# Optimization experiments

Hardware: AMD Instinct MI355X
Metric: run time of the kernel (lower is better)

Reference implementation:

```python
import jax, jax.numpy as jnp
import numpy as np

H = 8          # num heads
DK = 64        # d_model // H
D_MODEL = 512
WIN = 256


def setup_inputs() -> dict:
    key = jax.random.key(0)
    ks = jax.random.split(key, 12)
    B, S = 2, 2048
    mk = lambda k, shape, s=1.0: jax.random.normal(k, shape, dtype=jnp.float32) * s
    inp = {
        "query": mk(ks[0], (B, S, D_MODEL)),
        "key_in": mk(ks[1], (B, S, D_MODEL)),
        "value": mk(ks[2], (B, S, D_MODEL)),
        # nn.Linear(d_model, d_model) weights (out,in) and biases, x4
        "Wq": mk(ks[3], (D_MODEL, D_MODEL), 0.02), "bq": jnp.zeros((D_MODEL,), jnp.float32),
        "Wk": mk(ks[4], (D_MODEL, D_MODEL), 0.02), "bk": jnp.zeros((D_MODEL,), jnp.float32),
        "Wv": mk(ks[5], (D_MODEL, D_MODEL), 0.02), "bv": jnp.zeros((D_MODEL,), jnp.float32),
        "Wo": mk(ks[6], (D_MODEL, D_MODEL), 0.02), "bo": jnp.zeros((D_MODEL,), jnp.float32),
    }
    return inp


def reference(query, key_in, value, Wq, bq, Wk, bk, Wv, bv, Wo, bo):
    B, S, D = query.shape
    scale = np.float32(1.0 / np.sqrt(DK))

    def proj(x, W, b):
        # (B,S,D) -> (B,H,S,DK)
        return (x @ W.T + b).reshape(B, S, H, DK).transpose(0, 2, 1, 3)

    q = proj(query, Wq, bq)
    k = proj(key_in, Wk, bk)
    v = proj(value, Wv, bv)

    # Faithful to naive_masked_matmul: full (B,H,S,S) scores, with entries
    # OUTSIDE the sliding window left at exactly 0.0 (NOT -inf) before softmax.
    scores = jnp.einsum('bhid,bhjd->bhij', q, k) * scale
    idx = jnp.arange(S)
    band = jnp.abs(idx[:, None] - idx[None, :]) <= (WIN // 2)  # (S,S) bool
    scores = jnp.where(band, scores, jnp.float32(0.0))

    p_attn = jax.nn.softmax(scores, axis=-1)
    x = jnp.einsum('bhij,bhjd->bhid', p_attn, v)          # (B,H,S,DK)
    x = x.transpose(0, 2, 1, 3).reshape(B, S, D)          # (B,S,D)
    return x @ Wo.T + bo
```

## Files before the change

kernel.cpp:

```cpp
#include <hip/hip_runtime.h>
#include <hip/hip_bf16.h>

#define SS 2048
#define DD 512
#define HWIN 128

typedef __bf16 bf16x8 __attribute__((ext_vector_type(8)));
typedef unsigned short u16x8 __attribute__((ext_vector_type(8)));
typedef float f32x4 __attribute__((ext_vector_type(4)));

__device__ __forceinline__ unsigned short f2bf(float x) {
    unsigned u = __builtin_bit_cast(unsigned, x);
    return (unsigned short)((u + 0x7fffu + ((u >> 16) & 1u)) >> 16);
}
__device__ __forceinline__ float bf2f(unsigned short s) {
    unsigned u = ((unsigned)s) << 16;
    return __builtin_bit_cast(float, u);
}
__device__ __forceinline__ void split_bf(float x, unsigned short& h, unsigned short& l) {
    h = f2bf(x);
    l = f2bf(x - bf2f(h));
}
__device__ __forceinline__ void split8(float4 f0, float4 f1, u16x8& h, u16x8& l) {
    const float vals[8] = {f0.x, f0.y, f0.z, f0.w, f1.x, f1.y, f1.z, f1.w};
    #pragma unroll
    for (int i = 0; i < 8; ++i) {
        unsigned short hh, ll;
        split_bf(vals[i], hh, ll);
        h[i] = hh;
        l[i] = ll;
    }
}
__device__ __forceinline__ f32x4 mfma16(u16x8 a, u16x8 b, f32x4 c) {
    return __builtin_amdgcn_mfma_f32_16x16x32_bf16(
        __builtin_bit_cast(bf16x8, a), __builtin_bit_cast(bf16x8, b), c, 0, 0, 0);
}

template <bool A_FP32, bool OUT_SPLIT>
__device__ __forceinline__ void gemm_split_body(
    const float* __restrict__ Af,
    const unsigned short* __restrict__ AHg, const unsigned short* __restrict__ ALg,
    const float* __restrict__ W, const float* __restrict__ bias,
    unsigned short* __restrict__ OH, unsigned short* __restrict__ OL,
    float* __restrict__ OF)
{
    constexpr int K = 512, N = 512;
    __shared__ unsigned short Ah[8 * 64 * 8], Al[8 * 64 * 8];
    __shared__ unsigned short Bh[4 * 64 * 8], Bl[4 * 64 * 8];

    const int tid = threadIdx.x, wave = tid >> 6, lane = tid & 63;
    const int lm = lane & 15, lq = lane >> 4;
    const int m0 = blockIdx.y * 128, n0 = blockIdx.x * 64;
    const int wm = wave >> 1, wn = wave & 1;

    f32x4 acc[4][2] = {};

    const int ar0 = m0 + (wave * 2 + 0) * 16 + lm;
    const int ar1 = m0 + (wave * 2 + 1) * 16 + lm;
    const int br  = n0 + wave * 16 + lm;
    const int kb  = lq * 8;

    unsigned short* aD0h = &Ah[((wave * 2 + 0) * 64 + lane) * 8];
    unsigned short* aD1h = &Ah[((wave * 2 + 1) * 64 + lane) * 8];
    unsigned short* aD0l = &Al[((wave * 2 + 0) * 64 + lane) * 8];
    unsigned short* aD1l = &Al[((wave * 2 + 1) * 64 + lane) * 8];
    unsigned short* bDh  = &Bh[(wave * 64 + lane) * 8];
    unsigned short* bDl  = &Bl[(wave * 64 + lane) * 8];

    for (int k0 = 0; k0 < K; k0 += 32) {
        u16x8 a0h, a0l, a1h, a1l, b0h, b0l;
        if (A_FP32) {
            const float* p0 = Af + (size_t)ar0 * K + k0 + kb;
            split8(*(const float4*)p0, *(const float4*)(p0 + 4), a0h, a0l);
            const float* p1 = Af + (size_t)ar1 * K + k0 + kb;
            split8(*(const float4*)p1, *(const float4*)(p1 + 4), a1h, a1l);
        } else {
            a0h = *(const u16x8*)(AHg + (size_t)ar0 * K + k0 + kb);
            a0l = *(const u16x8*)(ALg + (size_t)ar0 * K + k0 + kb);
            a1h = *(const u16x8*)(AHg + (size_t)ar1 * K + k0 + kb);
            a1l = *(const u16x8*)(ALg + (size_t)ar1 * K + k0 + kb);
        }
        {
            const float* pw = W + (size_t)br * K + k0 + kb;
            split8(*(const float4*)pw, *(const float4*)(pw + 4), b0h, b0l);
        }
        __syncthreads();
        *(u16x8*)aD0h = a0h; *(u16x8*)aD0l = a0l;
        *(u16x8*)aD1h = a1h; *(u16x8*)aD1l = a1l;
        *(u16x8*)bDh  = b0h; *(u16x8*)bDl  = b0l;
        __syncthreads();

        u16x8 afh[4], afl[4], bfh[2], bfl[2];
        #pragma unroll
        for (int i = 0; i < 4; ++i) {
            afh[i] = *(const u16x8*)&Ah[((wm * 4 + i) * 64 + lane) * 8];
            afl[i] = *(const u16x8*)&Al[((wm * 4 + i) * 64 + lane) * 8];
        }
        #pragma unroll
        for (int j = 0; j < 2; ++j) {
            bfh[j] = *(const u16x8*)&Bh[((wn * 2 + j) * 64 + lane) * 8];
            bfl[j] = *(const u16x8*)&Bl[((wn * 2 + j) * 64 + lane) * 8];
        }
        #pragma unroll
        for (int i = 0; i < 4; ++i)
            #pragma unroll
            for (int j = 0; j < 2; ++j) {
                acc[i][j] = mfma16(afh[i], bfh[j], acc[i][j]);
                acc[i][j] = mfma16(afh[i], bfl[j], acc[i][j]);
                acc[i][j] = mfma16(afl[i], bfh[j], acc[i][j]);
            }
    }

    #pragma unroll
    for (int i = 0; i < 4; ++i)
        #pragma unroll
        for (int j = 0; j < 2; ++j) {
            const int col = n0 + (wn * 2 + j) * 16 + lm;
            const float bv = bias[col];
            #pragma unroll
            for (int r = 0; r < 4; ++r) {
                const int row = m0 + (wm * 4 + i) * 16 + lq * 4 + r;
                const float v = acc[i][j][r] + bv;
                if (OUT_SPLIT) {
                    unsigned short h, l;
                    split_bf(v, h, l);
                    OH[(size_t)row * N + col] = h;
                    OL[(size_t)row * N + col] = l;
                } else {
                    OF[(size_t)row * N + col] = v;
                }
            }
        }
}

__global__ __launch_bounds__(256) void proj_gemm(
    const float* __restrict__ q, const float* __restrict__ k, const float* __restrict__ v,
    const float* __restrict__ Wq, const float* __restrict__ Wk, const float* __restrict__ Wv,
    const float* __restrict__ bq, const float* __restrict__ bk, const float* __restrict__ bv,
    unsigned short* __restrict__ base)
{
    const int z = blockIdx.z;
    const float* A = (z == 0) ? q : ((z == 1) ? k : v);
    const float* W = (z == 0) ? Wq : ((z == 1) ? Wk : Wv);
    const float* bias = (z == 0) ? bq : ((z == 1) ? bk : bv);
    unsigned short* OH = base + (size_t)z * 4194304;
    unsigned short* OL = OH + 2097152;
    gemm_split_body<true, true>(A, nullptr, nullptr, W, bias, OH, OL, nullptr);
}

__global__ __launch_bounds__(256) void out_gemm(
    const unsigned short* __restrict__ XH, const unsigned short* __restrict__ XL,
    const float* __restrict__ Wo, const float* __restrict__ bo, float* __restrict__ O)
{
    gemm_split_body<false, false>(nullptr, XH, XL, Wo, bo, nullptr, nullptr, O);
}

__global__ __launch_bounds__(256) void vsum_stage1(
    const unsigned short* __restrict__ VH, const unsigned short* __restrict__ VL,
    float* __restrict__ partial)
{
    const int bh = blockIdx.x, c = blockIdx.y;
    const int h = bh & 7, b = bh >> 3;
    const int t = threadIdx.x, d = t & 63, g = t >> 6;
    __shared__ float p[4][64];
    const size_t base = ((size_t)b * SS + c * 64) * DD + (size_t)h * 64 + d;
    float acc = 0.f;
    #pragma unroll 4
    for (int s = g; s < 64; s += 4) {
        const size_t ix = base + (size_t)s * DD;
        acc += bf2f(VH[ix]) + bf2f(VL[ix]);
    }
    p[g][d] = acc;
    __syncthreads();
    if (t < 64)
        partial[((size_t)bh * 32 + c) * 64 + t] =
            p[0][t] + p[1][t] + p[2][t] + p[3][t];
}

__global__ __launch_bounds__(64) void vsum_stage2(
    const float* __restrict__ partial, float* __restrict__ VS)
{
    const int bh = blockIdx.x, d = threadIdx.x;
    float acc = 0.f;
    #pragma unroll 8
    for (int c = 0; c < 32; ++c)
        acc += partial[((size_t)bh * 32 + c) * 64 + d];
    VS[bh * 64 + d] = acc;
}

__global__ __launch_bounds__(256) void attn_mfma(
    const unsigned short* __restrict__ QH, const unsigned short* __restrict__ QL,
    const unsigned short* __restrict__ KH, const unsigned short* __restrict__ KL,
    const unsigned short* __restrict__ VH, const unsigned short* __restrict__ VL,
    const float* __restrict__ VS,
    unsigned short* __restrict__ XH, unsigned short* __restrict__ XL)
{
    const int bh = blockIdx.y, h = bh & 7, b = bh >> 3;
    const int i0 = blockIdx.x * 64;
    const int tid = threadIdx.x, wave = tid >> 6, lane = tid & 63;
    const int lm = lane & 15, lq = lane >> 4;
    const int kb = lq * 8;

    __shared__ unsigned short Kth[64][72], Ktl[64][72];
    __shared__ unsigned short Vth[64][72], Vtl[64][72];
    __shared__ unsigned short Swh[64][72], Swl[64][72];

    const size_t qoff = ((size_t)(b * SS + i0 + wave * 16 + lm)) * DD + h * 64 + kb;
    const u16x8 aQ0h = *(const u16x8*)(QH + qoff);
    const u16x8 aQ0l = *(const u16x8*)(QL + qoff);
    const u16x8 aQ1h = *(const u16x8*)(QH + qoff + 32);
    const u16x8 aQ1l = *(const u16x8*)(QL + qoff + 32);

    f32x4 oacc[4] = {};
    float dacc[4] = {0.f, 0.f, 0.f, 0.f};

    const int sr = tid & 63, sc = (tid >> 6) * 16;

    for (int jt = 0; jt < 5; ++jt) {
        const int jt0 = i0 - 128 + jt * 64;
        {
            const int j = jt0 + sr;
            u16x8 z = {0,0,0,0,0,0,0,0};
            u16x8 kh0 = z, kh1 = z, kl0 = z, kl1 = z;
            u16x8 vh0 = z, vh1 = z, vl0 = z, vl1 = z;
            if (j >= 0 && j < SS) {
                const size_t gb = ((size_t)(b * SS + j)) * DD + h * 64 + sc;
                kh0 = *(const u16x8*)(KH + gb); kh1 = *(const u16x8*)(KH + gb + 8);
                kl0 = *(const u16x8*)(KL + gb); kl1 = *(const u16x8*)(KL + gb + 8);
                vh0 = *(const u16x8*)(VH + gb); vh1 = *(const u16x8*)(VH + gb + 8);
                vl0 = *(const u16x8*)(VL + gb); vl1 = *(const u16x8*)(VL + gb + 8);
            }
            *(u16x8*)&Kth[sr][sc]     = kh0; *(u16x8*)&Kth[sr][sc + 8] = kh1;
            *(u16x8*)&Ktl[sr][sc]     = kl0; *(u16x8*)&Ktl[sr][sc + 8] = kl1;
            #pragma unroll
            for (int cc = 0; cc < 8; ++cc) {
                Vth[sc + cc][sr] = vh0[cc]; Vth[sc + 8 + cc][sr] = vh1[cc];
                Vtl[sc + cc][sr] = vl0[cc]; Vtl[sc + 8 + cc][sr] = vl1[cc];
            }
        }
        __syncthreads();

        #pragma unroll
        for (int js = 0; js < 4; ++js) {
            const int j0 = js * 16;
            const u16x8 bK0h = *(const u16x8*)&Kth[j0 + lm][kb];
            const u16x8 bK0l = *(const u16x8*)&Ktl[j0 + lm][kb];
            const u16x8 bK1h = *(const u16x8*)&Kth[j0 + lm][kb + 32];
            const u16x8 bK1l = *(const u16x8*)&Ktl[j0 + lm][kb + 32];
            f32x4 s = {0.f, 0.f, 0.f, 0.f};
            s = mfma16(aQ0h, bK0h, s);
            s = mfma16(aQ0h, bK0l, s);
            s = mfma16(aQ0l, bK0h, s);
            s = mfma16(aQ1h, bK1h, s);
            s = mfma16(aQ1h, bK1l, s);
            s = mfma16(aQ1l, bK1h, s);
            const int jg = jt0 + j0 + lm;
            const int iq = i0 + wave * 16 + lq * 4;
            #pragma unroll
            for (int r = 0; r < 4; ++r) {
                const int qi = iq + r;
                const bool in = (jg >= 0) && (jg < SS) &&
                                (jg >= qi - HWIN) && (jg <= qi + HWIN);
                const float w = in ? (__expf(s[r] * 0.125f) - 1.0f) : 0.0f;
                dacc[r] += w;
                unsigned short wh, wl;
                split_bf(w, wh, wl);
                Swh[wave * 16 + lq * 4 + r][j0 + lm] = wh;
                Swl[wave * 16 + lq * 4 + r][j0 + lm] = wl;
            }
        }
        __syncthreads();

        const u16x8 aP0h = *(const u16x8*)&Swh[wave * 16 + lm][kb];
        const u16x8 aP0l = *(const u16x8*)&Swl[wave * 16 + lm][kb];
        const u16x8 aP1h = *(const u16x8*)&Swh[wave * 16 + lm][kb + 32];
        const u16x8 aP1l = *(const u16x8*)&Swl[wave * 16 + lm][kb + 32];
        #pragma unroll
        for (int s4 = 0; s4 < 4; ++s4) {
            const u16x8 bV0h = *(const u16x8*)&Vth[s4 * 16 + lm][kb];
            const u16x8 bV0l = *(const u16x8*)&Vtl[s4 * 16 + lm][kb];
            const u16x8 bV1h = *(const u16x8*)&Vth[s4 * 16 + lm][kb + 32];
            const u16x8 bV1l = *(const u16x8*)&Vtl[s4 * 16 + lm][kb + 32];
            oacc[s4] = mfma16(aP0h, bV0h, oacc[s4]);
            oacc[s4] = mfma16(aP0l, bV0h, oacc[s4]);
            oacc[s4] = mfma16(aP0h, bV0l, oacc[s4]);
            oacc[s4] = mfma16(aP1h, bV1h, oacc[s4]);
            oacc[s4] = mfma16(aP1l, bV1h, oacc[s4]);
            oacc[s4] = mfma16(aP1h, bV1l, oacc[s4]);
        }
        __syncthreads();
    }

    #pragma unroll
    for (int r = 0; r < 4; ++r) {
        float v = dacc[r];
        v += __shfl_xor(v, 1);
        v += __shfl_xor(v, 2);
        v += __shfl_xor(v, 4);
        v += __shfl_xor(v, 8);
        dacc[r] = v + 2048.0f;
    }

    #pragma unroll
    for (int s4 = 0; s4 < 4; ++s4) {
        const float vsv = VS[bh * 64 + s4 * 16 + lm];
        #pragma unroll
        for (int r = 0; r < 4; ++r) {
            const int qrow = i0 + wave * 16 + lq * 4 + r;
            const float x = (oacc[s4][r] + vsv) / dacc[r];
            unsigned short xh, xl;
            split_bf(x, xh, xl);
            const size_t ix = ((size_t)(b * SS + qrow)) * DD + h * 64 + s4 * 16 + lm;
            XH[ix] = xh;
            XL[ix] = xl;
        }
    }
}

extern "C" void kernel_launch(void* const* d_in, const int* in_sizes, int n_in,
                              void* d_out, int out_size, void* d_ws, size_t ws_size,
                              hipStream_t stream)
{
    const float* query  = (const float*)d_in[0];
    const float* key_in = (const float*)d_in[1];
    const float* value  = (const float*)d_in[2];
    const float* Wq = (const float*)d_in[3]; const float* bq = (const float*)d_in[4];
    const float* Wk = (const float*)d_in[5]; const float* bk = (const float*)d_in[6];
    const float* Wv = (const float*)d_in[7]; const float* bv = (const float*)d_in[8];
    const float* Wo = (const float*)d_in[9]; const float* bo = (const float*)d_in[10];

    unsigned short* wsb = (unsigned short*)d_ws;
    unsigned short* QH = wsb;
    unsigned short* QL = wsb + 2097152;
    unsigned short* KH = wsb + 4194304;
    unsigned short* KL = wsb + 6291456;
    unsigned short* VH = wsb + 8388608;
    unsigned short* VL = wsb + 10485760;
    unsigned short* XH = wsb + 12582912;
    unsigned short* XL = wsb + 14680064;
    float* VSp = (float*)((char*)d_ws + 33554432);
    float* part = (float*)XH;

    proj_gemm<<<dim3(8, 32, 3), 256, 0, stream>>>(
        query, key_in, value, Wq, Wk, Wv, bq, bk, bv, QH);

    vsum_stage1<<<dim3(16, 32), 256, 0, stream>>>(VH, VL, part);
    vsum_stage2<<<16, 64, 0, stream>>>(part, VSp);

    attn_mfma<<<dim3(32, 16), 256, 0, stream>>>(
        QH, QL, KH, KL, VH, VL, VSp, XH, XL);

    out_gemm<<<dim3(8, 32), 256, 0, stream>>>(XH, XL, Wo, bo, (float*)d_out);
}
```

Before: 177.4 us.

## Pre-split projection weights once and remap block indices for XCD locality

Adds a castW kernel that splits Wq/Wk/Wv into interleaved bf16 hi/lo pairs once per call, so the projection GEMM loads pre-split weights instead of re-splitting fp32 weights in every block. All GEMM and attention launches move to flat 1D grids with an index remap that groups blocks sharing a weight tile or (batch, head) onto the same XCD via the round-robin dispatch, improving L2 reuse. This adds an extra kernel launch and workspace traffic, and relocates the partial-sum buffer inside the workspace.

Result: no change. 177.1 us (-0.1%).

```diff
diff --git a/kernel.cpp b/kernel.cpp
--- a/kernel.cpp
+++ b/kernel.cpp
@@ -36,13 +36,29 @@
         __builtin_bit_cast(bf16x8, a), __builtin_bit_cast(bf16x8, b), c, 0, 0, 0);
 }
 
-template <bool A_FP32, bool OUT_SPLIT>
+__global__ __launch_bounds__(256) void castW(
+    const float* __restrict__ wq, const float* __restrict__ wk,
+    const float* __restrict__ wv, unsigned short* __restrict__ dst)
+{
+    const size_t e0 = ((size_t)blockIdx.x * 256 + threadIdx.x) * 8;
+    const float* src; size_t off;
+    if      (e0 < 262144) { src = wq; off = e0; }
+    else if (e0 < 524288) { src = wk; off = e0 - 262144; }
+    else                  { src = wv; off = e0 - 524288; }
+    u16x8 h, l;
+    split8(*(const float4*)(src + off), *(const float4*)(src + off + 4), h, l);
+    *(u16x8*)(dst + 2 * e0)     = h;
+    *(u16x8*)(dst + 2 * e0 + 8) = l;
+}
+
+template <bool A_FP32, bool B_PAIRED, bool OUT_SPLIT>
 __device__ __forceinline__ void gemm_split_body(
     const float* __restrict__ Af,
     const unsigned short* __restrict__ AHg, const unsigned short* __restrict__ ALg,
-    const float* __restrict__ W, const float* __restrict__ bias,
+    const unsigned short* __restrict__ Wp, const float* __restrict__ Wf,
+    const float* __restrict__ bias,
     unsigned short* __restrict__ OH, unsigned short* __restrict__ OL,
-    float* __restrict__ OF)
+    float* __restrict__ OF, int m0, int n0)
 {
     constexpr int K = 512, N = 512;
     __shared__ unsigned short Ah[8 * 64 * 8], Al[8 * 64 * 8];
@@ -50,7 +66,6 @@
 
     const int tid = threadIdx.x, wave = tid >> 6, lane = tid & 63;
     const int lm = lane & 15, lq = lane >> 4;
-    const int m0 = blockIdx.y * 128, n0 = blockIdx.x * 64;
     const int wm = wave >> 1, wn = wave & 1;
 
     f32x4 acc[4][2] = {};
@@ -80,8 +95,12 @@
             a1h = *(const u16x8*)(AHg + (size_t)ar1 * K + k0 + kb);
             a1l = *(const u16x8*)(ALg + (size_t)ar1 * K + k0 + kb);
         }
-        {
-            const float* pw = W + (size_t)br * K + k0 + kb;
+        if (B_PAIRED) {
+            const unsigned short* pw = Wp + 2 * ((size_t)br * K + k0 + kb);
+            b0h = *(const u16x8*)pw;
+            b0l = *(const u16x8*)(pw + 8);
+        } else {
+            const float* pw = Wf + (size_t)br * K + k0 + kb;
             split8(*(const float4*)pw, *(const float4*)(pw + 4), b0h, b0l);
         }
         __syncthreads();
@@ -135,24 +154,35 @@
 
 __global__ __launch_bounds__(256) void proj_gemm(
     const float* __restrict__ q, const float* __restrict__ k, const float* __restrict__ v,
-    const float* __restrict__ Wq, const float* __restrict__ Wk, const float* __restrict__ Wv,
+    const unsigned short* __restrict__ WP,
     const float* __restrict__ bq, const float* __restrict__ bk, const float* __restrict__ bv,
     unsigned short* __restrict__ base)
 {
-    const int z = blockIdx.z;
+    const int d = blockIdx.x;
+    const int hi = d >> 6, low = d & 63;
+    const int x = low >> 3, r = low & 7;
+    const int g = hi * 8 + r;
+    const int y = g / 3, z = g - y * 3;
+
     const float* A = (z == 0) ? q : ((z == 1) ? k : v);
-    const float* W = (z == 0) ? Wq : ((z == 1) ? Wk : Wv);
+    const unsigned short* Wp = WP + (size_t)z * 524288;
     const float* bias = (z == 0) ? bq : ((z == 1) ? bk : bv);
     unsigned short* OH = base + (size_t)z * 4194304;
     unsigned short* OL = OH + 2097152;
-    gemm_split_body<true, true>(A, nullptr, nullptr, W, bias, OH, OL, nullptr);
+    gemm_split_body<true, true, true>(A, nullptr, nullptr, Wp, nullptr, bias,
+                                      OH, OL, nullptr, y * 128, x * 64);
 }
 
 __global__ __launch_bounds__(256) void out_gemm(
     const unsigned short* __restrict__ XH, const unsigned short* __restrict__ XL,
     const float* __restrict__ Wo, const float* __restrict__ bo, float* __restrict__ O)
 {
-    gemm_split_body<false, false>(nullptr, XH, XL, Wo, bo, nullptr, nullptr, O);
+    const int d = blockIdx.x;
+    const int hi = d >> 6, low = d & 63;
+    const int x = low >> 3, r = low & 7;
+    const int y = hi * 8 + r;
+    gemm_split_body<false, false, false>(nullptr, XH, XL, nullptr, Wo, bo,
+                                         nullptr, nullptr, O, y * 128, x * 64);
 }
 
 __global__ __launch_bounds__(256) void vsum_stage1(
@@ -195,8 +225,12 @@
     const float* __restrict__ VS,
     unsigned short* __restrict__ XH, unsigned short* __restrict__ XL)
 {
-    const int bh = blockIdx.y, h = bh & 7, b = bh >> 3;
-    const int i0 = blockIdx.x * 64;
+    const int dblk = blockIdx.x;
+    const int bhi = dblk >> 8, blow = dblk & 255;
+    const int xblk = blow >> 3, rr = blow & 7;
+    const int bh = bhi * 8 + rr;
+    const int h = bh & 7, b = bh >> 3;
+    const int i0 = xblk * 64;
     const int tid = threadIdx.x, wave = tid >> 6, lane = tid & 63;
     const int lm = lane & 15, lq = lane >> 4;
     const int kb = lq * 8;
@@ -339,16 +373,19 @@
     unsigned short* XH = wsb + 12582912;
     unsigned short* XL = wsb + 14680064;
     float* VSp = (float*)((char*)d_ws + 33554432);
-    float* part = (float*)XH;
-
-    proj_gemm<<<dim3(8, 32, 3), 256, 0, stream>>>(
-        query, key_in, value, Wq, Wk, Wv, bq, bk, bv, QH);
+    unsigned short* WP = XH;
+    float* part = (float*)(wsb + 14155776);
+
+    castW<<<384, 256, 0, stream>>>(Wq, Wk, Wv, WP);
+
+    proj_gemm<<<768, 256, 0, stream>>>(
+        query, key_in, value, WP, bq, bk, bv, QH);
 
     vsum_stage1<<<dim3(16, 32), 256, 0, stream>>>(VH, VL, part);
     vsum_stage2<<<16, 64, 0, stream>>>(part, VSp);
 
-    attn_mfma<<<dim3(32, 16), 256, 0, stream>>>(
+    attn_mfma<<<512, 256, 0, stream>>>(
         QH, QL, KH, KL, VH, VL, VSp, XH, XL);
 
-    out_gemm<<<dim3(8, 32), 256, 0, stream>>>(XH, XL, Wo, bo, (float*)d_out);
-}
+    out_gemm<<<256, 256, 0, stream>>>(XH, XL, Wo, bo, (float*)d_out);
+}
```

## Pre-split weights once, drop LDS staging in GEMMs, remap block indices

Applied to the files above, without the earlier changes.

Adds a castW kernel that converts all four weight matrices to interleaved bf16 hi/lo pairs, so the projection and output GEMMs no longer re-split the weights in every tile. Both GEMMs are rewritten without shared memory: each wave loads its A and B fragments directly from global memory and computes a 32x64 tile. Blocks use a 1D grid with a remapped index, and the attention grid is also swizzled, which is meant to improve L2 locality across neighbouring blocks. The cost is one extra kernel launch plus more redundant global and L2 traffic, since fragments are no longer shared between waves through LDS.

Result: slower. 208.6 us (+17.6%).

```diff
diff --git a/kernel.cpp b/kernel.cpp
--- a/kernel.cpp
+++ b/kernel.cpp
@@ -36,123 +36,191 @@
         __builtin_bit_cast(bf16x8, a), __builtin_bit_cast(bf16x8, b), c, 0, 0, 0);
 }
 
-template <bool A_FP32, bool OUT_SPLIT>
-__device__ __forceinline__ void gemm_split_body(
-    const float* __restrict__ Af,
-    const unsigned short* __restrict__ AHg, const unsigned short* __restrict__ ALg,
-    const float* __restrict__ W, const float* __restrict__ bias,
-    unsigned short* __restrict__ OH, unsigned short* __restrict__ OL,
-    float* __restrict__ OF)
-{
-    constexpr int K = 512, N = 512;
-    __shared__ unsigned short Ah[8 * 64 * 8], Al[8 * 64 * 8];
-    __shared__ unsigned short Bh[4 * 64 * 8], Bl[4 * 64 * 8];
-
-    const int tid = threadIdx.x, wave = tid >> 6, lane = tid & 63;
-    const int lm = lane & 15, lq = lane >> 4;
-    const int m0 = blockIdx.y * 128, n0 = blockIdx.x * 64;
-    const int wm = wave >> 1, wn = wave & 1;
-
-    f32x4 acc[4][2] = {};
-
-    const int ar0 = m0 + (wave * 2 + 0) * 16 + lm;
-    const int ar1 = m0 + (wave * 2 + 1) * 16 + lm;
-    const int br  = n0 + wave * 16 + lm;
-    const int kb  = lq * 8;
-
-    unsigned short* aD0h = &Ah[((wave * 2 + 0) * 64 + lane) * 8];
-    unsigned short* aD1h = &Ah[((wave * 2 + 1) * 64 + lane) * 8];
-    unsigned short* aD0l = &Al[((wave * 2 + 0) * 64 + lane) * 8];
-    unsigned short* aD1l = &Al[((wave * 2 + 1) * 64 + lane) * 8];
-    unsigned short* bDh  = &Bh[(wave * 64 + lane) * 8];
-    unsigned short* bDl  = &Bl[(wave * 64 + lane) * 8];
-
-    for (int k0 = 0; k0 < K; k0 += 32) {
-        u16x8 a0h, a0l, a1h, a1l, b0h, b0l;
-        if (A_FP32) {
-            const float* p0 = Af + (size_t)ar0 * K + k0 + kb;
-            split8(*(const float4*)p0, *(const float4*)(p0 + 4), a0h, a0l);
-            const float* p1 = Af + (size_t)ar1 * K + k0 + kb;
-            split8(*(const float4*)p1, *(const float4*)(p1 + 4), a1h, a1l);
-        } else {
-            a0h = *(const u16x8*)(AHg + (size_t)ar0 * K + k0 + kb);
-            a0l = *(const u16x8*)(ALg + (size_t)ar0 * K + k0 + kb);
-            a1h = *(const u16x8*)(AHg + (size_t)ar1 * K + k0 + kb);
-            a1l = *(const u16x8*)(ALg + (size_t)ar1 * K + k0 + kb);
-        }
-        {
-            const float* pw = W + (size_t)br * K + k0 + kb;
-            split8(*(const float4*)pw, *(const float4*)(pw + 4), b0h, b0l);
-        }
-        __syncthreads();
-        *(u16x8*)aD0h = a0h; *(u16x8*)aD0l = a0l;
-        *(u16x8*)aD1h = a1h; *(u16x8*)aD1l = a1l;
-        *(u16x8*)bDh  = b0h; *(u16x8*)bDl  = b0l;
-        __syncthreads();
-
-        u16x8 afh[4], afl[4], bfh[2], bfl[2];
-        #pragma unroll
-        for (int i = 0; i < 4; ++i) {
-            afh[i] = *(const u16x8*)&Ah[((wm * 4 + i) * 64 + lane) * 8];
-            afl[i] = *(const u16x8*)&Al[((wm * 4 + i) * 64 + lane) * 8];
-        }
-        #pragma unroll
-        for (int j = 0; j < 2; ++j) {
-            bfh[j] = *(const u16x8*)&Bh[((wn * 2 + j) * 64 + lane) * 8];
-            bfl[j] = *(const u16x8*)&Bl[((wn * 2 + j) * 64 + lane) * 8];
-        }
-        #pragma unroll
-        for (int i = 0; i < 4; ++i)
-            #pragma unroll
-            for (int j = 0; j < 2; ++j) {
-                acc[i][j] = mfma16(afh[i], bfh[j], acc[i][j]);
-                acc[i][j] = mfma16(afh[i], bfl[j], acc[i][j]);
-                acc[i][j] = mfma16(afl[i], bfh[j], acc[i][j]);
-            }
-    }
-
-    #pragma unroll
-    for (int i = 0; i < 4; ++i)
-        #pragma unroll
-        for (int j = 0; j < 2; ++j) {
-            const int col = n0 + (wn * 2 + j) * 16 + lm;
-            const float bv = bias[col];
-            #pragma unroll
-            for (int r = 0; r < 4; ++r) {
-                const int row = m0 + (wm * 4 + i) * 16 + lq * 4 + r;
-                const float v = acc[i][j][r] + bv;
-                if (OUT_SPLIT) {
-                    unsigned short h, l;
-                    split_bf(v, h, l);
-                    OH[(size_t)row * N + col] = h;
-                    OL[(size_t)row * N + col] = l;
-                } else {
-                    OF[(size_t)row * N + col] = v;
-                }
-            }
-        }
-}
+__global__ __launch_bounds__(256) void castW(
+    const float* __restrict__ wq, const float* __restrict__ wk,
+    const float* __restrict__ wv, const float* __restrict__ wo,
+    unsigned short* __restrict__ WP, unsigned short* __restrict__ WoP)
+{
+    const size_t e0 = ((size_t)blockIdx.x * 256 + threadIdx.x) * 8;
+    const float* src; size_t off; unsigned short* dst;
+    if      (e0 < 262144) { src = wq; off = e0;          dst = WP + 2 * e0; }
+    else if (e0 < 524288) { src = wk; off = e0 - 262144; dst = WP + 2 * e0; }
+    else if (e0 < 786432) { src = wv; off = e0 - 524288; dst = WP + 2 * e0; }
+    else                  { src = wo; off = e0 - 786432; dst = WoP + 2 * (e0 - 786432); }
+    u16x8 h, l;
+    split8(*(const float4*)(src + off), *(const float4*)(src + off + 4), h, l);
+    *(u16x8*)(dst)     = h;
+    *(u16x8*)(dst + 8) = l;
+}
+
 
 __global__ __launch_bounds__(256) void proj_gemm(
     const float* __restrict__ q, const float* __restrict__ k, const float* __restrict__ v,
-    const float* __restrict__ Wq, const float* __restrict__ Wk, const float* __restrict__ Wv,
+    const unsigned short* __restrict__ WP,
     const float* __restrict__ bq, const float* __restrict__ bk, const float* __restrict__ bv,
     unsigned short* __restrict__ base)
 {
-    const int z = blockIdx.z;
+    const int g = blockIdx.x;
+    const int u = ((g >> 6) << 3) | (g & 7);
+    const int nblk = (g >> 3) & 7;
+    const int z = u >> 5, mblk = u & 31;
+
     const float* A = (z == 0) ? q : ((z == 1) ? k : v);
-    const float* W = (z == 0) ? Wq : ((z == 1) ? Wk : Wv);
+    const unsigned short* Wp = WP + (size_t)z * 524288;
     const float* bias = (z == 0) ? bq : ((z == 1) ? bk : bv);
     unsigned short* OH = base + (size_t)z * 4194304;
     unsigned short* OL = OH + 2097152;
-    gemm_split_body<true, true>(A, nullptr, nullptr, W, bias, OH, OL, nullptr);
+
+    const int m0 = mblk * 128, n0 = nblk * 64;
+    const int wave = threadIdx.x >> 6, lane = threadIdx.x & 63;
+    const int lm = lane & 15, lq = lane >> 4;
+    const int kb = lq * 8;
+    const int row0 = m0 + wave * 32 + lm;
+
+    f32x4 acc[2][4] = {};
+
+    const float* a0p = A + (size_t)row0 * 512 + kb;
+    const float* a1p = a0p + (size_t)16 * 512;
+    const unsigned short* bp0 = Wp + 2 * ((size_t)(n0 + 0 * 16 + lm) * 512 + kb);
+    const unsigned short* bp1 = Wp + 2 * ((size_t)(n0 + 1 * 16 + lm) * 512 + kb);
+    const unsigned short* bp2 = Wp + 2 * ((size_t)(n0 + 2 * 16 + lm) * 512 + kb);
+    const unsigned short* bp3 = Wp + 2 * ((size_t)(n0 + 3 * 16 + lm) * 512 + kb);
+
+    #pragma unroll 2
+    for (int k0 = 0; k0 < 512; k0 += 32) {
+        u16x8 a0h, a0l, a1h, a1l;
+        split8(*(const float4*)(a0p + k0), *(const float4*)(a0p + k0 + 4), a0h, a0l);
+        split8(*(const float4*)(a1p + k0), *(const float4*)(a1p + k0 + 4), a1h, a1l);
+        const unsigned short* bq0 = bp0 + 2 * k0;
+        const unsigned short* bq1 = bp1 + 2 * k0;
+        const unsigned short* bq2 = bp2 + 2 * k0;
+        const unsigned short* bq3 = bp3 + 2 * k0;
+        const u16x8 b0h = *(const u16x8*)(bq0), b0l = *(const u16x8*)(bq0 + 8);
+        const u16x8 b1h = *(const u16x8*)(bq1), b1l = *(const u16x8*)(bq1 + 8);
+        const u16x8 b2h = *(const u16x8*)(bq2), b2l = *(const u16x8*)(bq2 + 8);
+        const u16x8 b3h = *(const u16x8*)(bq3), b3l = *(const u16x8*)(bq3 + 8);
+
+        acc[0][0] = mfma16(a0h, b0h, acc[0][0]);
+        acc[0][0] = mfma16(a0h, b0l, acc[0][0]);
+        acc[0][0] = mfma16(a0l, b0h, acc[0][0]);
+        acc[0][1] = mfma16(a0h, b1h, acc[0][1]);
+        acc[0][1] = mfma16(a0h, b1l, acc[0][1]);
+        acc[0][1] = mfma16(a0l, b1h, acc[0][1]);
+        acc[0][2] = mfma16(a0h, b2h, acc[0][2]);
+        acc[0][2] = mfma16(a0h, b2l, acc[0][2]);
+        acc[0][2] = mfma16(a0l, b2h, acc[0][2]);
+        acc[0][3] = mfma16(a0h, b3h, acc[0][3]);
+        acc[0][3] = mfma16(a0h, b3l, acc[0][3]);
+        acc[0][3] = mfma16(a0l, b3h, acc[0][3]);
+        acc[1][0] = mfma16(a1h, b0h, acc[1][0]);
+        acc[1][0] = mfma16(a1h, b0l, acc[1][0]);
+        acc[1][0] = mfma16(a1l, b0h, acc[1][0]);
+        acc[1][1] = mfma16(a1h, b1h, acc[1][1]);
+        acc[1][1] = mfma16(a1h, b1l, acc[1][1]);
+        acc[1][1] = mfma16(a1l, b1h, acc[1][1]);
+        acc[1][2] = mfma16(a1h, b2h, acc[1][2]);
+        acc[1][2] = mfma16(a1h, b2l, acc[1][2]);
+        acc[1][2] = mfma16(a1l, b2h, acc[1][2]);
+        acc[1][3] = mfma16(a1h, b3h, acc[1][3]);
+        acc[1][3] = mfma16(a1h, b3l, acc[1][3]);
+        acc[1][3] = mfma16(a1l, b3h, acc[1][3]);
+    }
+
+    #pragma unroll
+    for (int t = 0; t < 2; ++t)
+        #pragma unroll
+        for (int j = 0; j < 4; ++j) {
+            const int col = n0 + j * 16 + lm;
+            const float bv_ = bias[col];
+            #pragma unroll
+            for (int r = 0; r < 4; ++r) {
+                const int row = m0 + wave * 32 + t * 16 + lq * 4 + r;
+                const float vv = acc[t][j][r] + bv_;
+                unsigned short hh, ll;
+                split_bf(vv, hh, ll);
+                OH[(size_t)row * 512 + col] = hh;
+                OL[(size_t)row * 512 + col] = ll;
+            }
+        }
 }
 
 __global__ __launch_bounds__(256) void out_gemm(
-    const unsigned short* __restrict__ XH, const unsigned short* __restrict__ XL,
-    const float* __restrict__ Wo, const float* __restrict__ bo, float* __restrict__ O)
-{
-    gemm_split_body<false, false>(nullptr, XH, XL, Wo, bo, nullptr, nullptr, O);
+    const unsigned short* __restrict__ XHg, const unsigned short* __restrict__ XLg,
+    const unsigned short* __restrict__ WoP, const float* __restrict__ bo,
+    float* __restrict__ O)
+{
+    const int g = blockIdx.x;
+    const int u = ((g >> 6) << 3) | (g & 7);
+    const int nblk = (g >> 3) & 7;
+
+    const int m0 = u * 128, n0 = nblk * 64;
+    const int wave = threadIdx.x >> 6, lane = threadIdx.x & 63;
+    const int lm = lane & 15, lq = lane >> 4;
+    const int kb = lq * 8;
+    const int row0 = m0 + wave * 32 + lm;
+
+    f32x4 acc[2][4] = {};
+
+    const unsigned short* xh0 = XHg + (size_t)row0 * 512 + kb;
+    const unsigned short* xl0 = XLg + (size_t)row0 * 512 + kb;
+    const unsigned short* xh1 = xh0 + (size_t)16 * 512;
+    const unsigned short* xl1 = xl0 + (size_t)16 * 512;
+    const unsigned short* bp0 = WoP + 2 * ((size_t)(n0 + 0 * 16 + lm) * 512 + kb);
+    const unsigned short* bp1 = WoP + 2 * ((size_t)(n0 + 1 * 16 + lm) * 512 + kb);
+    const unsigned short* bp2 = WoP + 2 * ((size_t)(n0 + 2 * 16 + lm) * 512 + kb);
+    const unsigned short* bp3 = WoP + 2 * ((size_t)(n0 + 3 * 16 + lm) * 512 + kb);
+
+    #pragma unroll 2
+    for (int k0 = 0; k0 < 512; k0 += 32) {
+        const u16x8 a0h = *(const u16x8*)(xh0 + k0), a0l = *(const u16x8*)(xl0 + k0);
+        const u16x8 a1h = *(const u16x8*)(xh1 + k0), a1l = *(const u16x8*)(xl1 + k0);
+        const unsigned short* bq0 = bp0 + 2 * k0;
+        const unsigned short* bq1 = bp1 + 2 * k0;
+        const unsigned short* bq2 = bp2 + 2 * k0;
+        const unsigned short* bq3 = bp3 + 2 * k0;
+        const u16x8 b0h = *(const u16x8*)(bq0), b0l = *(const u16x8*)(bq0 + 8);
+        const u16x8 b1h = *(const u16x8*)(bq1), b1l = *(const u16x8*)(bq1 + 8);
+        const u16x8 b2h = *(const u16x8*)(bq2), b2l = *(const u16x8*)(bq2 + 8);
+        const u16x8 b3h = *(const u16x8*)(bq3), b3l = *(const u16x8*)(bq3 + 8);
+
+        acc[0][0] = mfma16(a0h, b0h, acc[0][0]);
+        acc[0][0] = mfma16(a0h, b0l, acc[0][0]);
+        acc[0][0] = mfma16(a0l, b0h, acc[0][0]);
+        acc[0][1] = mfma16(a0h, b1h, acc[0][1]);
+        acc[0][1] = mfma16(a0h, b1l, acc[0][1]);
+        acc[0][1] = mfma16(a0l, b1h, acc[0][1]);
+        acc[0][2] = mfma16(a0h, b2h, acc[0][2]);
+        acc[0][2] = mfma16(a0h, b2l, acc[0][2]);
+        acc[0][2] = mfma16(a0l, b2h, acc[0][2]);
+        acc[0][3] = mfma16(a0h, b3h, acc[0][3]);
+        acc[0][3] = mfma16(a0h, b3l, acc[0][3]);
+        acc[0][3] = mfma16(a0l, b3h, acc[0][3]);
+        acc[1][0] = mfma16(a1h, b0h, acc[1][0]);
+        acc[1][0] = mfma16(a1h, b0l, acc[1][0]);
+        acc[1][0] = mfma16(a1l, b0h, acc[1][0]);
+        acc[1][1] = mfma16(a1h, b1h, acc[1][1]);
+        acc[1][1] = mfma16(a1h, b1l, acc[1][1]);
+        acc[1][1] = mfma16(a1l, b1h, acc[1][1]);
+        acc[1][2] = mfma16(a1h, b2h, acc[1][2]);
+        acc[1][2] = mfma16(a1h, b2l, acc[1][2]);
+        acc[1][2] = mfma16(a1l, b2h, acc[1][2]);
+        acc[1][3] = mfma16(a1h, b3h, acc[1][3]);
+        acc[1][3] = mfma16(a1h, b3l, acc[1][3]);
+        acc[1][3] = mfma16(a1l, b3h, acc[1][3]);
+    }
+
+    #pragma unroll
+    for (int t = 0; t < 2; ++t)
+        #pragma unroll
+        for (int j = 0; j < 4; ++j) {
+            const int col = n0 + j * 16 + lm;
+            const float bv_ = bo[col];
+            #pragma unroll
+            for (int r = 0; r < 4; ++r) {
+                const int row = m0 + wave * 32 + t * 16 + lq * 4 + r;
+                O[(size_t)row * 512 + col] = acc[t][j][r] + bv_;
+            }
+        }
 }
 
 __global__ __launch_bounds__(256) void vsum_stage1(
@@ -195,8 +263,12 @@
     const float* __restrict__ VS,
     unsigned short* __restrict__ XH, unsigned short* __restrict__ XL)
 {
-    const int bh = blockIdx.y, h = bh & 7, b = bh >> 3;
-    const int i0 = blockIdx.x * 64;
+    const int dblk = blockIdx.x;
+    const int bhi = dblk >> 8, blow = dblk & 255;
+    const int xblk = blow >> 3, rr = blow & 7;
+    const int bh = bhi * 8 + rr;
+    const int h = bh & 7, b = bh >> 3;
+    const int i0 = xblk * 64;
     const int tid = threadIdx.x, wave = tid >> 6, lane = tid & 63;
     const int lm = lane & 15, lq = lane >> 4;
     const int kb = lq * 8;
@@ -338,17 +410,20 @@
     unsigned short* VL = wsb + 10485760;
     unsigned short* XH = wsb + 12582912;
     unsigned short* XL = wsb + 14680064;
-    float* VSp = (float*)((char*)d_ws + 33554432);
-    float* part = (float*)XH;
-
-    proj_gemm<<<dim3(8, 32, 3), 256, 0, stream>>>(
-        query, key_in, value, Wq, Wk, Wv, bq, bk, bv, QH);
+    unsigned short* WP  = wsb + 16777216;
+    unsigned short* WoP = wsb + 18350080;
+    float* part = (float*)((char*)d_ws + 62914560);
+    float* VSp  = (float*)((char*)d_ws + 63045632);
+
+    castW<<<512, 256, 0, stream>>>(Wq, Wk, Wv, Wo, WP, WoP);
+
+    proj_gemm<<<768, 256, 0, stream>>>(query, key_in, value, WP, bq, bk, bv, QH);
 
     vsum_stage1<<<dim3(16, 32), 256, 0, stream>>>(VH, VL, part);
     vsum_stage2<<<16, 64, 0, stream>>>(part, VSp);
 
-    attn_mfma<<<dim3(32, 16), 256, 0, stream>>>(
+    attn_mfma<<<512, 256, 0, stream>>>(
         QH, QL, KH, KL, VH, VL, VSp, XH, XL);
 
-    out_gemm<<<dim3(8, 32), 256, 0, stream>>>(XH, XL, Wo, bo, (float*)d_out);
-}
+    out_gemm<<<256, 256, 0, stream>>>(XH, XL, WoP, bo, (float*)d_out);
+}
```
